# Kernel tuning notes

Measured on AMD Instinct MI355X. Metric: run time of the kernel, lower is better.

## Reference

```python
import jax, jax.numpy as jnp
import numpy as np

N, E, D_IN, H, OUT = 50000, 800000, 128, 256, 2
BN_EPS = 1e-5
LN_EPS = 1e-5


def _xavier(k, fi, fo):
    lim = float(np.sqrt(6.0 / (fi + fo)))
    return jax.random.uniform(k, (fi, fo), minval=-lim, maxval=lim, dtype=jnp.float32)


def setup_inputs() -> dict:
    key = jax.random.key(0)
    ks = jax.random.split(key, 8)
    return {
        "x": jax.random.normal(ks[0], (N, D_IN), dtype=jnp.float32),
        "edge_index": jax.random.randint(ks[1], (2, E), 0, N, dtype=jnp.int32),
        "feature_scale": jnp.ones((D_IN,), jnp.float32),
        "feature_bias": jnp.zeros((D_IN,), jnp.float32),
        "bn0_g": jnp.ones((D_IN,), jnp.float32),
        "bn0_b": jnp.zeros((D_IN,), jnp.float32),
        "W1": _xavier(ks[2], D_IN, H), "b1": jnp.zeros((H,), jnp.float32),
        "bn1_g": jnp.ones((H,), jnp.float32), "bn1_b": jnp.zeros((H,), jnp.float32),
        "ln1_g": jnp.ones((H,), jnp.float32), "ln1_b": jnp.zeros((H,), jnp.float32),
        "W2": _xavier(ks[3], H, H), "b2": jnp.zeros((H,), jnp.float32),
        "bn2_g": jnp.ones((H,), jnp.float32), "bn2_b": jnp.zeros((H,), jnp.float32),
        "ln2_g": jnp.ones((H,), jnp.float32), "ln2_b": jnp.zeros((H,), jnp.float32),
        "Wout": _xavier(ks[4], H, OUT), "bout": jnp.zeros((OUT,), jnp.float32),
    }


def _batchnorm(x, g, b):
    # training-mode BatchNorm1d: batch stats over node axis, biased variance
    mu = jnp.mean(x, axis=0)
    var = jnp.mean(jnp.square(x - mu), axis=0)
    return g * (x - mu) * jax.lax.rsqrt(var + BN_EPS) + b


def _layernorm(x, g, b):
    mu = jnp.mean(x, axis=-1, keepdims=True)
    var = jnp.mean(jnp.square(x - mu), axis=-1, keepdims=True)
    return g * (x - mu) * jax.lax.rsqrt(var + LN_EPS) + b


def _gcn(x, W, b, src, dst, dinv):
    # PyG GCNConv with self-loops: D^{-1/2}(A+I)D^{-1/2} X W + b
    h = x @ W                                   # [N, F]
    norm = (dinv[src] * dinv[dst])[:, None]     # [E, 1]
    msg = h[src] * norm                         # [E, F] (dominant traffic)
    agg = jax.ops.segment_sum(msg, dst, num_segments=N)
    return agg + (dinv * dinv)[:, None] * h + b


def _forward(x, feature_scale, feature_bias, bn0_g, bn0_b,
             W1, b1, bn1_g, bn1_b, ln1_g, ln1_b,
             W2, b2, bn2_g, bn2_b, ln2_g, ln2_b,
             Wout, bout, edge_index):
    src, dst = edge_index[0], edge_index[1]
    deg = jax.ops.segment_sum(jnp.ones((E,), x.dtype), dst, num_segments=N) + 1.0
    dinv = jax.lax.rsqrt(deg)

    h = x * feature_scale + feature_bias
    h = _batchnorm(h, bn0_g, bn0_b)            # input_bn; dropout = identity (eval)

    # layer 0 (no residual: i == 0)
    h1 = _gcn(h, W1, b1, src, dst, dinv)
    h1 = jax.nn.relu(h1)
    h1 = _batchnorm(h1, bn1_g, bn1_b)
    h1 = _layernorm(h1, ln1_g, ln1_b)

    # layer 1 (residual add, shapes match)
    h2 = _gcn(h1, W2, b2, src, dst, dinv)
    h2 = jax.nn.relu(h2)
    h2 = _batchnorm(h2, bn2_g, bn2_b)
    h2 = _layernorm(h2, ln2_g, ln2_b)
    h2 = h2 + h1

    return h2 @ Wout + bout


def reference(x, edge_index, feature_scale, feature_bias, bn0_g, bn0_b,
              W1, b1, bn1_g, bn1_b, ln1_g, ln1_b,
              W2, b2, bn2_g, bn2_b, ln2_g, ln2_b,
              Wout, bout):
    return _forward(x, feature_scale, feature_bias, bn0_g, bn0_b,
                    W1, b1, bn1_g, bn1_b, ln1_g, ln1_b,
                    W2, b2, bn2_g, bn2_b, ln2_g, ln2_b,
                    Wout, bout, edge_index)
```

## Files before the change

kernel.cpp:

```cpp
#include <hip/hip_runtime.h>
#include <hip/hip_bf16.h>
#include <stdint.h>

#define N_NODES 50000
#define N_EDGES 800000
#define D_IN    128
#define H_DIM   256
#define BN_EPS  1e-5f
#define LN_EPS  1e-5f
#define NBLK2 782
#define SLICE_ELEMS ((size_t)N_NODES * 32)
#define EDGE_CHUNK 4096
#define BN0_BLOCKS 1024
#define TR_BLOCKS 256
#define NBKT 196
#define CHUNK 2048
#define RCHUNKS 391

typedef float v4f __attribute__((ext_vector_type(4)));
typedef float v2f __attribute__((ext_vector_type(2)));
typedef short v8s __attribute__((ext_vector_type(8)));
typedef unsigned v4u __attribute__((ext_vector_type(4)));

__device__ __forceinline__ float bflo(unsigned u){ return __uint_as_float(u << 16); }
__device__ __forceinline__ float bfhi(unsigned u){ return __uint_as_float(u & 0xffff0000u); }
__device__ __forceinline__ unsigned short f2bf(float f){
  unsigned u = __float_as_uint(f);
  u += 0x7fffu + ((u >> 16) & 1u);
  return (unsigned short)(u >> 16);
}
__device__ __forceinline__ unsigned pack2(float a, float b){
  return (unsigned)f2bf(a) | ((unsigned)f2bf(b) << 16);
}

__device__ __forceinline__ int block_excl_scan(int v){
  int t = threadIdx.x;
  int lane = t & 63, w = t >> 6;
  int inc = v;
  #pragma unroll
  for (int m = 1; m < 64; m <<= 1){
    int o = __shfl_up(inc, m, 64);
    if (lane >= m) inc += o;
  }
  __shared__ int wsum[4];
  if (lane == 63) wsum[w] = inc;
  __syncthreads();
  int base = 0;
  #pragma unroll
  for (int j = 0; j < 4; ++j) if (j < w) base += wsum[j];
  return base + inc - v;
}

__global__ __launch_bounds__(256) void bn0r1_k(const int* ei, const float* x,
                                               const float* fs, const float* fb,
                                               float* S, float* Q, int* ghist){
  int b = blockIdx.x, t = threadIdx.x;
  if (b >= BN0_BLOCKS){
    __shared__ int lh[NBKT];
    int b2 = b - BN0_BLOCKS;
    for (int i = t; i < NBKT; i += 256) lh[i] = 0;
    __syncthreads();
    int e0 = b2 * CHUNK;
    int n = min(CHUNK, N_EDGES - e0);
    for (int i = t; i < n; i += 256)
      atomicAdd(&lh[ei[N_EDGES + e0 + i] >> 8], 1);
    __syncthreads();
    if (t < NBKT && lh[t] > 0) atomicAdd(&ghist[t], lh[t]);
    return;
  }
  int cl = t & 31, rg = t >> 5;
  int c = cl * 4;
  float4 fs4 = *(const float4*)(fs + c);
  float4 fb4 = *(const float4*)(fb + c);
  float s0=0,s1=0,s2=0,s3=0,q0=0,q1=0,q2=0,q3=0;
  for (int row = b * 8 + rg; row < N_NODES; row += BN0_BLOCKS * 8){
    float4 xv = *(const float4*)(x + (size_t)row * D_IN + c);
    float v0 = xv.x * fs4.x + fb4.x;
    float v1 = xv.y * fs4.y + fb4.y;
    float v2 = xv.z * fs4.z + fb4.z;
    float v3 = xv.w * fs4.w + fb4.w;
    s0 += v0; s1 += v1; s2 += v2; s3 += v3;
    q0 += v0*v0; q1 += v1*v1; q2 += v2*v2; q3 += v3*v3;
  }
  __shared__ float red[256][8];
  red[t][0]=s0; red[t][1]=s1; red[t][2]=s2; red[t][3]=s3;
  red[t][4]=q0; red[t][5]=q1; red[t][6]=q2; red[t][7]=q3;
  __syncthreads();
  float* Sr = S + (b & 7) * D_IN;
  float* Qr = Q + (b & 7) * D_IN;
  if (t < 32){
    float a[8];
    #pragma unroll
    for (int i = 0; i < 8; ++i) a[i] = red[t][i];
    for (int j = 1; j < 8; ++j)
      #pragma unroll
      for (int i = 0; i < 8; ++i) a[i] += red[t + 32*j][i];
    #pragma unroll
    for (int i = 0; i < 4; ++i){ atomicAdd(&Sr[t*4+i], a[i]); atomicAdd(&Qr[t*4+i], a[4+i]); }
  }
}

__global__ __launch_bounds__(256) void r3_k(const int* ei, const int* ghist, int* gcursor, unsigned* ebuf){
  __shared__ unsigned short dstS[CHUNK];
  __shared__ int lh[NBKT], cb[NBKT], sbb[NBKT];
  int t = threadIdx.x;
  int v = (t < NBKT) ? ghist[t] : 0;
  int epre = block_excl_scan(v);
  if (t < NBKT){ sbb[t] = epre; lh[t] = 0; }
  __syncthreads();
  int e0 = blockIdx.x * CHUNK;
  int n = min(CHUNK, N_EDGES - e0);
  for (int i = t; i < n; i += 256){
    int d = ei[N_EDGES + e0 + i];
    dstS[i] = (unsigned short)d;
    atomicAdd(&lh[d >> 8], 1);
  }
  __syncthreads();
  if (t < NBKT && lh[t] > 0) cb[t] = sbb[t] + atomicAdd(&gcursor[t], lh[t]);
  __syncthreads();
  if (t < NBKT) lh[t] = 0;
  __syncthreads();
  for (int i = t; i < n; i += 256){
    int d = dstS[i];
    int bkt = d >> 8;
    int r = atomicAdd(&lh[bkt], 1);
    unsigned src = (unsigned)ei[e0 + i];
    ebuf[cb[bkt] + r] = ((unsigned)(d & 255) << 16) | src;
  }
}

__global__ __launch_bounds__(256) void sortprep_k(const unsigned* ebuf, const int* ghist,
                                                  int* perm, int* offs, float* dinv,
                                                  unsigned short* edges,
                                                  const float* W1, const float* W2,
                                                  unsigned short* W1t, unsigned short* W2t){
  int b = blockIdx.x, t = threadIdx.x;
  if (b < NBKT){
    __shared__ int h[256], dh[128], ep_s[128], W_s[128], lc[128], curs[256], sbb[NBKT + 1];
    int gv = (t < NBKT) ? ghist[t] : 0;
    int gpre = block_excl_scan(gv);
    if (t < NBKT) sbb[t] = gpre;
    if (t == NBKT - 1) sbb[NBKT] = gpre + gv;
    h[t] = 0;
    if (t < 128){ dh[t] = 0; lc[t] = 0; }
    __syncthreads();
    int lo = sbb[b], hi = sbb[b + 1];
    for (int i = lo + t; i < hi; i += 256)
      atomicAdd(&h[(ebuf[i] >> 16) & 255], 1);
    __syncthreads();
    int node = b * 256 + t;
    bool valid = node < N_NODES;
    int deg = valid ? h[t] : 0;
    if (valid) atomicAdd(&dh[min(deg, 127)], 1);
    __syncthreads();
    int cv = (t < 128) ? dh[t] : 0;
    int e1 = block_excl_scan(cv);
    __syncthreads();
    int e2 = block_excl_scan((t < 128) ? cv * t : 0);
    __syncthreads();
    if (t < 128){ ep_s[t] = e1; W_s[t] = e2; }
    __syncthreads();
    if (valid){
      int bin = min(deg, 127);
      int r = atomicAdd(&lc[bin], 1);
      int pl = ep_s[bin] + r;
      int pos = b * 256 + pl;
      int off = lo + W_s[bin] + (pl - ep_s[bin]) * deg;
      perm[pos] = node;
      offs[pos] = off;
      dinv[node] = rsqrtf((float)deg + 1.0f);
      curs[t] = off;
    }
    __syncthreads();
    for (int i = lo + t; i < hi; i += 256){
      unsigned u = ebuf[i];
      int l8 = (u >> 16) & 255;
      int pos = atomicAdd(&curs[l8], 1);
      edges[pos] = (unsigned short)(u & 0xffffu);
    }
    if (b == 0 && t == 0) offs[N_NODES] = N_EDGES;
    return;
  }
  int i = (b - NBKT) * 256 + t;
  if (i < D_IN * H_DIM){
    int r = i / H_DIM, c = i % H_DIM;
    W1t[c * D_IN + r] = f2bf(W1[i]);
  }
  if (i < H_DIM * H_DIM){
    int r = i / H_DIM, c = i % H_DIM;
    W2t[c * H_DIM + r] = f2bf(W2[i]);
  }
}

__global__ __launch_bounds__(256) void gemm1_k(const float* x, const float* S, const float* Q,
                                               const float* fs, const float* fb,
                                               const float* gg, const float* bb,
                                               const unsigned short* Bt, const float* dinv,
                                               unsigned short* C, int M){
  __shared__ __align__(16) short smem[18944];
  __shared__ float ac[128], cc[128], dvs[64];
  short* As = smem;
  short* Bs = smem + 64 * 136;
  int t = threadIdx.x;
  int m0 = blockIdx.x * 64;
  int lane = t & 63, w = t >> 6;
  int fr = lane & 15, quad = lane >> 4;
  if (t < 64) dvs[t] = (m0 + t < M) ? dinv[m0 + t] : 0.0f;
  if (t < 128){
    float s8 = 0.f, q8 = 0.f;
    #pragma unroll
    for (int rep = 0; rep < 8; ++rep){ s8 += S[rep * D_IN + t]; q8 += Q[rep * D_IN + t]; }
    const float invN = 1.0f / N_NODES;
    float mu = s8 * invN;
    float rs = rsqrtf(q8 * invN - mu * mu + BN_EPS);
    float a = gg[t] * rs * fs[t];
    ac[t] = a;
    cc[t] = gg[t] * rs * (fb[t] - mu) + bb[t];
  }
  __syncthreads();
  {
    int r = t >> 2, q = t & 3;
    int arow = m0 + r;
    #pragma unroll
    for (int j = 0; j < 4; ++j){
      int c = q * 32 + j * 8;
      float4 xv0 = {0,0,0,0}, xv1 = {0,0,0,0};
      if (arow < M){
        xv0 = *(const float4*)(x + (size_t)arow * D_IN + c);
        xv1 = *(const float4*)(x + (size_t)arow * D_IN + c + 4);
      }
      float4 a0 = *(const float4*)(&ac[c]);
      float4 a1 = *(const float4*)(&ac[c + 4]);
      float4 c0 = *(const float4*)(&cc[c]);
      float4 c1 = *(const float4*)(&cc[c + 4]);
      uint4 o;
      o.x = pack2(a0.x * xv0.x + c0.x, a0.y * xv0.y + c0.y);
      o.y = pack2(a0.z * xv0.z + c0.z, a0.w * xv0.w + c0.w);
      o.z = pack2(a1.x * xv1.x + c1.x, a1.y * xv1.y + c1.y);
      o.w = pack2(a1.z * xv1.z + c1.z, a1.w * xv1.w + c1.w);
      *(uint4*)(&As[r * 136 + c]) = o;
    }
  }
  v4f acc[4][4] = {};
  int sr = t >> 2;
  int sk = (t & 3) << 3;
  for (int k0 = 0; k0 < D_IN; k0 += 32){
    __syncthreads();
    #pragma unroll
    for (int j = 0; j < 4; ++j){
      int brow = sr + 64 * j;
      uint4 bv = *(const uint4*)(Bt + (size_t)brow * D_IN + k0 + sk);
      *(uint4*)(&Bs[brow * 40 + sk]) = bv;
    }
    __syncthreads();
    v8s af[4], bf[4];
    #pragma unroll
    for (int mi = 0; mi < 4; ++mi)
      af[mi] = *(const v8s*)(&As[(mi * 16 + fr) * 136 + k0 + quad * 8]);
    #pragma unroll
    for (int ni = 0; ni < 4; ++ni)
      bf[ni] = *(const v8s*)(&Bs[(w * 64 + ni * 16 + fr) * 40 + quad * 8]);
    #pragma unroll
    for (int mi = 0; mi < 4; ++mi)
      #pragma unroll
      for (int ni = 0; ni < 4; ++ni)
        acc[mi][ni] = __builtin_amdgcn_mfma_f32_16x16x32_bf16(af[mi], bf[ni], acc[mi][ni], 0, 0, 0);
  }
  __syncthreads();
  short* Cs = smem;
  #pragma unroll
  for (int mi = 0; mi < 4; ++mi)
    #pragma unroll
    for (int ni = 0; ni < 4; ++ni)
      #pragma unroll
      for (int r = 0; r < 4; ++r){
        int row = mi * 16 + quad * 4 + r;
        int col = w * 64 + ni * 16 + fr;
        Cs[row * 264 + col] = (short)f2bf(acc[mi][ni][r] * dvs[row]);
      }
  __syncthreads();
  int orow = t >> 2;
  int grow = m0 + orow;
  if (grow < M){
    #pragma unroll
    for (int j = 0; j < 4; ++j){
      int oc = (t & 3) * 16 + 64 * j;
      v8s v0 = *(const v8s*)(&Cs[orow * 264 + oc]);
      v8s v1 = *(const v8s*)(&Cs[orow * 264 + oc + 8]);
      *(v8s*)(&C[(size_t)(oc >> 5) * SLICE_ELEMS + (size_t)grow * 32 + (oc & 31)]) = v0;
      int oc1 = oc + 8;
      *(v8s*)(&C[(size_t)(oc1 >> 5) * SLICE_ELEMS + (size_t)grow * 32 + (oc1 & 31)]) = v1;
    }
  }
}

__global__ __launch_bounds__(256) void gemm2_k(const unsigned short* gB,
                                               const float* Sg, const float* Qg,
                                               const float* bng, const float* bnb,
                                               const float* lng, const float* lnb,
                                               const unsigned short* Bt, const float* dinv,
                                               unsigned short* C, unsigned short* h1, int M){
  __shared__ __align__(16) short smem[16896];
  __shared__ float scs[256], shs[256], lgs[256], lbs[256], muS[64], rsS[64], dvs[64];
  short* As = smem;
  short* Bs = smem + 64 * 40;
  int t = threadIdx.x;
  int m0 = blockIdx.x * 64;
  int lane = t & 63, w = t >> 6;
  int fr = lane & 15, quad = lane >> 4;
  if (t < 64) dvs[t] = (m0 + t < M) ? dinv[m0 + t] : 0.0f;
  {
    const float invN = 1.0f / N_NODES;
    float mu = Sg[t] * invN;
    float rs = rsqrtf(Qg[t] * invN - mu * mu + BN_EPS);
    float s = bng[t] * rs;
    scs[t] = s; shs[t] = bnb[t] - s * mu;
    lgs[t] = lng[t]; lbs[t] = lnb[t];
  }
  __syncthreads();
  {
    int r = t >> 2, q = t & 3;
    int grow = m0 + r;
    float sum = 0.f, sq = 0.f;
    if (grow < M){
      #pragma unroll
      for (int j = 0; j < 8; ++j){
        int c = q * 64 + j * 8;
        uint4 u = *(const uint4*)(gB + (size_t)grow * H_DIM + c);
        float4 s0 = *(const float4*)(&scs[c]);
        float4 s1 = *(const float4*)(&scs[c + 4]);
        float4 h0 = *(const float4*)(&shs[c]);
        float4 h4 = *(const float4*)(&shs[c + 4]);
        float v0 = s0.x * bflo(u.x) + h0.x;
        float v1 = s0.y * bfhi(u.x) + h0.y;
        float v2 = s0.z * bflo(u.y) + h0.z;
        float v3 = s0.w * bfhi(u.y) + h0.w;
        float v4 = s1.x * bflo(u.z) + h4.x;
        float v5 = s1.y * bfhi(u.z) + h4.y;
        float v6 = s1.z * bflo(u.w) + h4.z;
        float v7 = s1.w * bfhi(u.w) + h4.w;
        sum += v0+v1+v2+v3+v4+v5+v6+v7;
        sq  += v0*v0+v1*v1+v2*v2+v3*v3+v4*v4+v5*v5+v6*v6+v7*v7;
      }
    }
    sum += __shfl_xor(sum, 1, 64); sum += __shfl_xor(sum, 2, 64);
    sq  += __shfl_xor(sq, 1, 64);  sq  += __shfl_xor(sq, 2, 64);
    if (q == 0){
      float mu = sum * (1.0f / H_DIM);
      float var = sq * (1.0f / H_DIM) - mu * mu;
      muS[r] = mu;
      rsS[r] = rsqrtf(var + LN_EPS);
    }
  }
  v4f acc[4][4] = {};
  int sr = t >> 2;
  int sk = (t & 3) << 3;
  for (int k0 = 0; k0 < H_DIM; k0 += 32){
    __syncthreads();
    {
      int arow = m0 + sr;
      uint4 av = {0,0,0,0};
      if (arow < M){
        int c = k0 + sk;
        uint4 u = *(const uint4*)(gB + (size_t)arow * H_DIM + c);
        float mu = muS[sr], rs = rsS[sr];
        float4 s0 = *(const float4*)(&scs[c]);
        float4 s1 = *(const float4*)(&scs[c + 4]);
        float4 h0 = *(const float4*)(&shs[c]);
        float4 h4 = *(const float4*)(&shs[c + 4]);
        float4 g0 = *(const float4*)(&lgs[c]);
        float4 g1 = *(const float4*)(&lgs[c + 4]);
        float4 b0 = *(const float4*)(&lbs[c]);
        float4 b1 = *(const float4*)(&lbs[c + 4]);
        float y0 = g0.x * ((s0.x * bflo(u.x) + h0.x) - mu) * rs + b0.x;
        float y1 = g0.y * ((s0.y * bfhi(u.x) + h0.y) - mu) * rs + b0.y;
        float y2 = g0.z * ((s0.z * bflo(u.y) + h0.z) - mu) * rs + b0.z;
        float y3 = g0.w * ((s0.w * bfhi(u.y) + h0.w) - mu) * rs + b0.w;
        float y4 = g1.x * ((s1.x * bflo(u.z) + h4.x) - mu) * rs + b1.x;
        float y5 = g1.y * ((s1.y * bfhi(u.z) + h4.y) - mu) * rs + b1.y;
        float y6 = g1.z * ((s1.z * bflo(u.w) + h4.z) - mu) * rs + b1.z;
        float y7 = g1.w * ((s1.w * bfhi(u.w) + h4.w) - mu) * rs + b1.w;
        av.x = pack2(y0, y1); av.y = pack2(y2, y3);
        av.z = pack2(y4, y5); av.w = pack2(y6, y7);
        *(uint4*)(h1 + (size_t)arow * H_DIM + c) = av;
      }
      *(uint4*)(&As[sr * 40 + sk]) = av;
    }
    #pragma unroll
    for (int j = 0; j < 4; ++j){
      int brow = sr + 64 * j;
      uint4 bv = *(const uint4*)(Bt + (size_t)brow * H_DIM + k0 + sk);
      *(uint4*)(&Bs[brow * 40 + sk]) = bv;
    }
    __syncthreads();
    v8s af[4], bf[4];
    #pragma unroll
    for (int mi = 0; mi < 4; ++mi)
      af[mi] = *(const v8s*)(&As[(mi * 16 + fr) * 40 + quad * 8]);
    #pragma unroll
    for (int ni = 0; ni < 4; ++ni)
      bf[ni] = *(const v8s*)(&Bs[(w * 64 + ni * 16 + fr) * 40 + quad * 8]);
    #pragma unroll
    for (int mi = 0; mi < 4; ++mi)
      #pragma unroll
      for (int ni = 0; ni < 4; ++ni)
        acc[mi][ni] = __builtin_amdgcn_mfma_f32_16x16x32_bf16(af[mi], bf[ni], acc[mi][ni], 0, 0, 0);
  }
  __syncthreads();
  short* Cs = smem;
  #pragma unroll
  for (int mi = 0; mi < 4; ++mi)
    #pragma unroll
    for (int ni = 0; ni < 4; ++ni)
      #pragma unroll
      for (int r = 0; r < 4; ++r){
        int row = mi * 16 + quad * 4 + r;
        int col = w * 64 + ni * 16 + fr;
        Cs[row * 264 + col] = (short)f2bf(acc[mi][ni][r] * dvs[row]);
      }
  __syncthreads();
  int orow = t >> 2;
  int grow = m0 + orow;
  if (grow < M){
    #pragma unroll
    for (int j = 0; j < 4; ++j){
      int oc = (t & 3) * 16 + 64 * j;
      v8s v0 = *(const v8s*)(&Cs[orow * 264 + oc]);
      v8s v1 = *(const v8s*)(&Cs[orow * 264 + oc + 8]);
      *(v8s*)(&C[(size_t)(oc >> 5) * SLICE_ELEMS + (size_t)grow * 32 + (oc & 31)]) = v0;
      int oc1 = oc + 8;
      *(v8s*)(&C[(size_t)(oc1 >> 5) * SLICE_ELEMS + (size_t)grow * 32 + (oc1 & 31)]) = v1;
    }
  }
}

#define ACCP(u, A) { v2f d_ = {bflo(u), bfhi(u)}; A += d_; }
#define ACC8(vv) ACCP(vv.x, A0) ACCP(vv.y, A1) ACCP(vv.z, A2) ACCP(vv.w, A3)

__global__ __launch_bounds__(256, 4) void agg_k(const unsigned short* hs, const int* offsets,
                                                const unsigned short* edges, const int* perm,
                                                const float* dinv, const float* bias,
                                                unsigned short* g, float* Sg, float* Qg){
  __shared__ unsigned eds32[EDGE_CHUNK / 2];
  __shared__ float wps[4][4][16];
  int t = threadIdx.x;
  int lane = t & 63;
  int wv = t >> 6;
  int slice = blockIdx.x & 7;
  int l4 = lane & 3;
  int grp = blockIdx.x >> 3;
  int nb = grp * 64;
  int idx = nb + (t >> 2);
  int lastn = min(nb + 64, N_NODES);
  int blk0 = offsets[nb];
  int base = blk0 & ~1;
  int blkN = offsets[lastn];
  const unsigned* gsrc = (const unsigned*)(edges + base);
  int nu = min((blkN - base + 1) >> 1, EDGE_CHUNK / 2);
  for (int i = t; i < nu; i += 256)
    eds32[i] = gsrc[i];
  __syncthreads();
  bool act = idx < N_NODES;
  int node = act ? perm[idx] : 0;
  float dvv = act ? dinv[node] : 0.f;
  const uint4* hb4 = (const uint4*)(hs + (size_t)slice * SLICE_ELEMS);
  float4 bb0 = *(const float4*)(bias + slice * 32 + l4 * 8);
  float4 bb1 = *(const float4*)(bias + slice * 32 + l4 * 8 + 4);
  uint4 sv = hb4[(size_t)node * 4 + l4];
  v2f A0 = {bflo(sv.x), bfhi(sv.x)};
  v2f A1 = {bflo(sv.y), bfhi(sv.y)};
  v2f A2 = {bflo(sv.z), bfhi(sv.z)};
  v2f A3 = {bflo(sv.w), bfhi(sv.w)};
  int e  = act ? offsets[idx] : 0;
  int e1 = act ? offsets[idx + 1] : 0;
  if ((e & 1) && e < e1){
    int ru = (e - base) >> 1;
    unsigned d = (ru < EDGE_CHUNK / 2) ? eds32[ru] : gsrc[ru];
    uint4 vv = hb4[(size_t)(d >> 16) * 4 + l4];
    ACC8(vv);
    ++e;
  }
  for (; e + 16 <= e1; e += 16){
    int ru = (e - base) >> 1;
    unsigned dd[8];
    if (ru + 8 <= EDGE_CHUNK / 2){
      #pragma unroll
      for (int j = 0; j < 8; ++j) dd[j] = eds32[ru + j];
    } else {
      #pragma unroll
      for (int j = 0; j < 8; ++j) dd[j] = gsrc[ru + j];
    }
    uint4 v[16];
    #pragma unroll
    for (int j = 0; j < 8; ++j){
      v[2*j]   = hb4[(size_t)(dd[j] & 0xffffu) * 4 + l4];
      v[2*j+1] = hb4[(size_t)(dd[j] >> 16)     * 4 + l4];
    }
    #pragma unroll
    for (int j = 0; j < 16; ++j){ ACC8(v[j]); }
  }
  if (e + 8 <= e1){
    int ru = (e - base) >> 1;
    unsigned dd[4];
    if (ru + 4 <= EDGE_CHUNK / 2){
      #pragma unroll
      for (int j = 0; j < 4; ++j) dd[j] = eds32[ru + j];
    } else {
      #pragma unroll
      for (int j = 0; j < 4; ++j) dd[j] = gsrc[ru + j];
    }
    uint4 v[8];
    #pragma unroll
    for (int j = 0; j < 4; ++j){
      v[2*j]   = hb4[(size_t)(dd[j] & 0xffffu) * 4 + l4];
      v[2*j+1] = hb4[(size_t)(dd[j] >> 16)     * 4 + l4];
    }
    #pragma unroll
    for (int j = 0; j < 8; ++j){ ACC8(v[j]); }
    e += 8;
  }
  if (e + 4 <= e1){
    int ru = (e - base) >> 1;
    unsigned dd0, dd1;
    if (ru + 2 <= EDGE_CHUNK / 2){
      dd0 = eds32[ru]; dd1 = eds32[ru + 1];
    } else {
      dd0 = gsrc[ru]; dd1 = gsrc[ru + 1];
    }
    uint4 v[4];
    v[0] = hb4[(size_t)(dd0 & 0xffffu) * 4 + l4];
    v[1] = hb4[(size_t)(dd0 >> 16)     * 4 + l4];
    v[2] = hb4[(size_t)(dd1 & 0xffffu) * 4 + l4];
    v[3] = hb4[(size_t)(dd1 >> 16)     * 4 + l4];
    #pragma unroll
    for (int j = 0; j < 4; ++j){ ACC8(v[j]); }
    e += 4;
  }
  for (; e < e1; ++e){
    int r = e - base;
    unsigned d = ((r >> 1) < EDGE_CHUNK / 2) ? eds32[r >> 1] : gsrc[r >> 1];
    unsigned s = (r & 1) ? (d >> 16) : (d & 0xffffu);
    uint4 vv = hb4[(size_t)s * 4 + l4];
    ACC8(vv);
  }
  float y0 = act ? fmaxf(dvv * A0.x + bb0.x, 0.f) : 0.f;
  float y1 = act ? fmaxf(dvv * A0.y + bb0.y, 0.f) : 0.f;
  float y2 = act ? fmaxf(dvv * A1.x + bb0.z, 0.f) : 0.f;
  float y3 = act ? fmaxf(dvv * A1.y + bb0.w, 0.f) : 0.f;
  float y4 = act ? fmaxf(dvv * A2.x + bb1.x, 0.f) : 0.f;
  float y5 = act ? fmaxf(dvv * A2.y + bb1.y, 0.f) : 0.f;
  float y6 = act ? fmaxf(dvv * A3.x + bb1.z, 0.f) : 0.f;
  float y7 = act ? fmaxf(dvv * A3.y + bb1.w, 0.f) : 0.f;
  if (act){
    v4u o;
    o.x = pack2(y0, y1); o.y = pack2(y2, y3);
    o.z = pack2(y4, y5); o.w = pack2(y6, y7);
    __builtin_nontemporal_store(o, (v4u*)(g + (size_t)node * H_DIM + slice * 32 + l4 * 8));
  }
  float q0 = y0*y0, q1 = y1*y1, q2 = y2*y2, q3 = y3*y3;
  float q4 = y4*y4, q5 = y5*y5, q6 = y6*y6, q7 = y7*y7;
  #pragma unroll
  for (int m = 4; m < 64; m <<= 1){
    y0 += __shfl_xor(y0, m, 64); y1 += __shfl_xor(y1, m, 64);
    y2 += __shfl_xor(y2, m, 64); y3 += __shfl_xor(y3, m, 64);
    y4 += __shfl_xor(y4, m, 64); y5 += __shfl_xor(y5, m, 64);
    y6 += __shfl_xor(y6, m, 64); y7 += __shfl_xor(y7, m, 64);
    q0 += __shfl_xor(q0, m, 64); q1 += __shfl_xor(q1, m, 64);
    q2 += __shfl_xor(q2, m, 64); q3 += __shfl_xor(q3, m, 64);
    q4 += __shfl_xor(q4, m, 64); q5 += __shfl_xor(q5, m, 64);
    q6 += __shfl_xor(q6, m, 64); q7 += __shfl_xor(q7, m, 64);
  }
  if (lane < 4){
    wps[wv][lane][0] = y0; wps[wv][lane][1] = y1; wps[wv][lane][2] = y2; wps[wv][lane][3] = y3;
    wps[wv][lane][4] = y4; wps[wv][lane][5] = y5; wps[wv][lane][6] = y6; wps[wv][lane][7] = y7;
    wps[wv][lane][8] = q0; wps[wv][lane][9] = q1; wps[wv][lane][10] = q2; wps[wv][lane][11] = q3;
    wps[wv][lane][12] = q4; wps[wv][lane][13] = q5; wps[wv][lane][14] = q6; wps[wv][lane][15] = q7;
  }
  __syncthreads();
  if (t < 64){
    int tl = t >> 4, ti = t & 15;
    float v = wps[0][tl][ti] + wps[1][tl][ti] + wps[2][tl][ti] + wps[3][tl][ti];
    int col32 = tl * 8 + (ti & 7);
    if (ti < 8) atomicAdd(&Sg[slice * 32 + col32], v);
    else        atomicAdd(&Qg[slice * 32 + col32], v);
  }
}

__global__ __launch_bounds__(256) void apply2_k(const unsigned short* g,
                                                const float* Sg, const float* Qg,
                                                const float* bng, const float* bnb,
                                                const float* lng, const float* lnb,
                                                const unsigned short* h1, const float* Wout,
                                                const float* bout, float* out){
  int t = threadIdx.x;
  int lane32 = t & 31;
  int row = blockIdx.x * 8 + (t >> 5);
  if (row >= N_NODES) return;
  int c = lane32 * 8;
  const float invN = 1.0f / N_NODES;
  float4 S0 = *(const float4*)(Sg + c), S1 = *(const float4*)(Sg + c + 4);
  float4 Q0 = *(const float4*)(Qg + c), Q1 = *(const float4*)(Qg + c + 4);
  float4 G0 = *(const float4*)(bng + c), G1 = *(const float4*)(bng + c + 4);
  float4 B0 = *(const float4*)(bnb + c), B1 = *(const float4*)(bnb + c + 4);
  float Sa[8] = {S0.x,S0.y,S0.z,S0.w,S1.x,S1.y,S1.z,S1.w};
  float Qa[8] = {Q0.x,Q0.y,Q0.z,Q0.w,Q1.x,Q1.y,Q1.z,Q1.w};
  float Ga[8] = {G0.x,G0.y,G0.z,G0.w,G1.x,G1.y,G1.z,G1.w};
  float Ba[8] = {B0.x,B0.y,B0.z,B0.w,B1.x,B1.y,B1.z,B1.w};
  float scv[8], shv[8];
  #pragma unroll
  for (int j = 0; j < 8; ++j){
    float mu = Sa[j] * invN;
    float rs = rsqrtf(Qa[j] * invN - mu * mu + BN_EPS);
    float s = Ga[j] * rs;
    scv[j] = s; shv[j] = Ba[j] - s * mu;
  }
  uint4 u = *(const uint4*)(g + (size_t)row * H_DIM + c);
  float v0 = scv[0] * bflo(u.x) + shv[0];
  float v1 = scv[1] * bfhi(u.x) + shv[1];
  float v2 = scv[2] * bflo(u.y) + shv[2];
  float v3 = scv[3] * bfhi(u.y) + shv[3];
  float v4 = scv[4] * bflo(u.z) + shv[4];
  float v5 = scv[5] * bfhi(u.z) + shv[5];
  float v6 = scv[6] * bflo(u.w) + shv[6];
  float v7 = scv[7] * bfhi(u.w) + shv[7];
  float sum = v0+v1+v2+v3+v4+v5+v6+v7;
  float sq  = v0*v0+v1*v1+v2*v2+v3*v3+v4*v4+v5*v5+v6*v6+v7*v7;
  #pragma unroll
  for (int m = 1; m < 32; m <<= 1){ sum += __shfl_xor(sum, m, 64); sq += __shfl_xor(sq, m, 64); }
  float mu = sum * (1.0f / H_DIM);
  float var = sq * (1.0f / H_DIM) - mu * mu;
  float rs = rsqrtf(var + LN_EPS);
  float4 g40 = *(const float4*)(lng + c);
  float4 g41 = *(const float4*)(lng + c + 4);
  float4 b40 = *(const float4*)(lnb + c);
  float4 b41 = *(const float4*)(lnb + c + 4);
  uint4 hr = *(const uint4*)(h1 + (size_t)row * H_DIM + c);
  float y0 = g40.x * (v0 - mu) * rs + b40.x + bflo(hr.x);
  float y1 = g40.y * (v1 - mu) * rs + b40.y + bfhi(hr.x);
  float y2 = g40.z * (v2 - mu) * rs + b40.z + bflo(hr.y);
  float y3 = g40.w * (v3 - mu) * rs + b40.w + bfhi(hr.y);
  float y4 = g41.x * (v4 - mu) * rs + b41.x + bflo(hr.z);
  float y5 = g41.y * (v5 - mu) * rs + b41.y + bfhi(hr.z);
  float y6 = g41.z * (v6 - mu) * rs + b41.z + bflo(hr.w);
  float y7 = g41.w * (v7 - mu) * rs + b41.w + bfhi(hr.w);
  float4 w0 = *(const float4*)(Wout + c * 2);
  float4 w1 = *(const float4*)(Wout + c * 2 + 4);
  float4 w2 = *(const float4*)(Wout + c * 2 + 8);
  float4 w3 = *(const float4*)(Wout + c * 2 + 12);
  float o0 = y0*w0.x + y1*w0.z + y2*w1.x + y3*w1.z + y4*w2.x + y5*w2.z + y6*w3.x + y7*w3.z;
  float o1 = y0*w0.y + y1*w0.w + y2*w1.y + y3*w1.w + y4*w2.y + y5*w2.w + y6*w3.y + y7*w3.w;
  #pragma unroll
  for (int m = 1; m < 32; m <<= 1){ o0 += __shfl_xor(o0, m, 64); o1 += __shfl_xor(o1, m, 64); }
  if (lane32 == 0){
    out[(size_t)row * 2 + 0] = o0 + bout[0];
    out[(size_t)row * 2 + 1] = o1 + bout[1];
  }
}

extern "C" void kernel_launch(void* const* d_in, const int* in_sizes, int n_in,
                              void* d_out, int out_size, void* d_ws, size_t ws_size,
                              hipStream_t stream) {
  const float* x    = (const float*)d_in[0];
  const int*   ei   = (const int*)d_in[1];
  const float* fs   = (const float*)d_in[2];
  const float* fb   = (const float*)d_in[3];
  const float* bn0g = (const float*)d_in[4];
  const float* bn0b = (const float*)d_in[5];
  const float* W1   = (const float*)d_in[6];
  const float* b1   = (const float*)d_in[7];
  const float* bn1g = (const float*)d_in[8];
  const float* bn1b = (const float*)d_in[9];
  const float* ln1g = (const float*)d_in[10];
  const float* ln1b = (const float*)d_in[11];
  const float* W2   = (const float*)d_in[12];
  const float* b2   = (const float*)d_in[13];
  const float* bn2g = (const float*)d_in[14];
  const float* bn2b = (const float*)d_in[15];
  const float* ln2g = (const float*)d_in[16];
  const float* ln2b = (const float*)d_in[17];
  const float* Wout = (const float*)d_in[18];
  const float* bout = (const float*)d_in[19];
  float* out = (float*)d_out;

  char* w = (char*)d_ws;
  float* bn0S  = (float*)(w + 0);
  float* bn0Q  = (float*)(w + 4096);
  int*   ghist  = (int*)(w + 8192);
  int*   gcursor= (int*)(w + 8976);
  float* Sg1   = (float*)(w + 9760);
  float* Qg1   = (float*)(w + 10784);
  float* Sg2   = (float*)(w + 11808);
  float* Qg2   = (float*)(w + 12832);
  const size_t ZERO_BYTES = 13856;
  float* dinv  = (float*)(w + 211584);
  int*   offs  = (int*)(w + 411584);
  int*   perm  = (int*)(w + 611712);
  unsigned short* edges = (unsigned short*)(w + 1011712);
  unsigned short* W1t  = (unsigned short*)(w + 15411712);
  unsigned short* W2t  = (unsigned short*)(w + 15477248);
  unsigned short* hlin = (unsigned short*)(w + 15608320);
  unsigned*       ebuf = (unsigned*)(w + 15608320);
  unsigned short* gbuf = (unsigned short*)(w + 41208320);
  unsigned short* h1   = (unsigned short*)(w + 66808320);

  (void)in_sizes; (void)n_in; (void)out_size; (void)ws_size;

  hipMemsetAsync(d_ws, 0, ZERO_BYTES, stream);

  bn0r1_k<<<BN0_BLOCKS + RCHUNKS, 256, 0, stream>>>(ei, x, fs, fb, bn0S, bn0Q, ghist);
  r3_k<<<RCHUNKS, 256, 0, stream>>>(ei, ghist, gcursor, ebuf);
  sortprep_k<<<NBKT + TR_BLOCKS, 256, 0, stream>>>(
      ebuf, ghist, perm, offs, dinv, edges, W1, W2, W1t, W2t);

  int ggrid = (N_NODES + 63) / 64;
  int agg_blocks = NBLK2 * 8;

  gemm1_k<<<ggrid, 256, 0, stream>>>(x, bn0S, bn0Q, fs, fb, bn0g, bn0b, W1t, dinv, hlin, N_NODES);
  agg_k<<<agg_blocks, 256, 0, stream>>>(hlin, offs, edges, perm, dinv, b1, gbuf, Sg1, Qg1);

  gemm2_k<<<ggrid, 256, 0, stream>>>(gbuf, Sg1, Qg1, bn1g, bn1b, ln1g, ln1b, W2t, dinv, hlin, h1, N_NODES);
  agg_k<<<agg_blocks, 256, 0, stream>>>(hlin, offs, edges, perm, dinv, b2, gbuf, Sg2, Qg2);
  apply2_k<<<(N_NODES + 7) / 8, 256, 0, stream>>>(gbuf, Sg2, Qg2, bn2g, bn2b, ln2g, ln2b, h1, Wout, bout, out);
}
```

Before: 334.6 us.

## Enlarge gemm1 tile to 128 rows with 8 waves and stream A per k-step

gemm1 now processes 128 rows per block with 512 threads arranged as a 2x4 wave grid. Each block loads W1 tiles once for twice as many rows, which halves B-operand traffic. The A operand (BN-normalized x) is converted per 32-wide k-chunk instead of staging the whole row up front, so shared memory shrinks. The epilogue writes the output in two 64-row halves through shared memory with wider contiguous stores. The cost is half as many blocks, which lowers occupancy, plus extra barriers in the epilogue.

```diff
diff --git a/kernel.cpp b/kernel.cpp
--- a/kernel.cpp
+++ b/kernel.cpp
@@ -192,21 +192,22 @@
   }
 }
 
-__global__ __launch_bounds__(256) void gemm1_k(const float* x, const float* S, const float* Q,
+__global__ __launch_bounds__(512) void gemm1_k(const float* x, const float* S, const float* Q,
                                                const float* fs, const float* fb,
                                                const float* gg, const float* bb,
                                                const unsigned short* Bt, const float* dinv,
                                                unsigned short* C, int M){
-  __shared__ __align__(16) short smem[18944];
-  __shared__ float ac[128], cc[128], dvs[64];
+  __shared__ __align__(16) short smem[16896];
+  __shared__ float ac[128], cc[128], dvs[128];
   short* As = smem;
-  short* Bs = smem + 64 * 136;
+  short* Bs = smem + 128 * 40;
   int t = threadIdx.x;
-  int m0 = blockIdx.x * 64;
+  int m0 = blockIdx.x * 128;
   int lane = t & 63, w = t >> 6;
+  int wr = w >> 2, wc = w & 3;
   int fr = lane & 15, quad = lane >> 4;
-  if (t < 64) dvs[t] = (m0 + t < M) ? dinv[m0 + t] : 0.0f;
   if (t < 128){
+    dvs[t] = (m0 + t < M) ? dinv[m0 + t] : 0.0f;
     float s8 = 0.f, q8 = 0.f;
     #pragma unroll
     for (int rep = 0; rep < 8; ++rep){ s8 += S[rep * D_IN + t]; q8 += Q[rep * D_IN + t]; }
@@ -218,12 +219,14 @@
     cc[t] = gg[t] * rs * (fb[t] - mu) + bb[t];
   }
   __syncthreads();
-  {
-    int r = t >> 2, q = t & 3;
-    int arow = m0 + r;
-    #pragma unroll
-    for (int j = 0; j < 4; ++j){
-      int c = q * 32 + j * 8;
+  v4f acc[4][4] = {};
+  int ar = t >> 2, aq = t & 3;
+  int br = t >> 1, bh = t & 1;
+  for (int k0 = 0; k0 < D_IN; k0 += 32){
+    __syncthreads();
+    {
+      int arow = m0 + ar;
+      int c = k0 + aq * 8;
       float4 xv0 = {0,0,0,0}, xv1 = {0,0,0,0};
       if (arow < M){
         xv0 = *(const float4*)(x + (size_t)arow * D_IN + c);
@@ -238,58 +241,59 @@
       o.y = pack2(a0.z * xv0.z + c0.z, a0.w * xv0.w + c0.w);
       o.z = pack2(a1.x * xv1.x + c1.x, a1.y * xv1.y + c1.y);
       o.w = pack2(a1.z * xv1.z + c1.z, a1.w * xv1.w + c1.w);
-      *(uint4*)(&As[r * 136 + c]) = o;
-    }
-  }
-  v4f acc[4][4] = {};
-  int sr = t >> 2;
-  int sk = (t & 3) << 3;
-  for (int k0 = 0; k0 < D_IN; k0 += 32){
-    __syncthreads();
-    #pragma unroll
-    for (int j = 0; j < 4; ++j){
-      int brow = sr + 64 * j;
-      uint4 bv = *(const uint4*)(Bt + (size_t)brow * D_IN + k0 + sk);
-      *(uint4*)(&Bs[brow * 40 + sk]) = bv;
+      *(uint4*)(&As[ar * 40 + aq * 8]) = o;
+    }
+    {
+      const unsigned short* bp = Bt + (size_t)br * D_IN + k0 + bh * 16;
+      uint4 b0 = *(const uint4*)(bp);
+      uint4 b1 = *(const uint4*)(bp + 8);
+      *(uint4*)(&Bs[br * 40 + bh * 16]) = b0;
+      *(uint4*)(&Bs[br * 40 + bh * 16 + 8]) = b1;
     }
     __syncthreads();
     v8s af[4], bf[4];
     #pragma unroll
     for (int mi = 0; mi < 4; ++mi)
-      af[mi] = *(const v8s*)(&As[(mi * 16 + fr) * 136 + k0 + quad * 8]);
+      af[mi] = *(const v8s*)(&As[(wr * 64 + mi * 16 + fr) * 40 + quad * 8]);
     #pragma unroll
     for (int ni = 0; ni < 4; ++ni)
-      bf[ni] = *(const v8s*)(&Bs[(w * 64 + ni * 16 + fr) * 40 + quad * 8]);
+      bf[ni] = *(const v8s*)(&Bs[(wc * 64 + ni * 16 + fr) * 40 + quad * 8]);
     #pragma unroll
     for (int mi = 0; mi < 4; ++mi)
       #pragma unroll
       for (int ni = 0; ni < 4; ++ni)
         acc[mi][ni] = __builtin_amdgcn_mfma_f32_16x16x32_bf16(af[mi], bf[ni], acc[mi][ni], 0, 0, 0);
   }
-  __syncthreads();
   short* Cs = smem;
   #pragma unroll
-  for (int mi = 0; mi < 4; ++mi)
-    #pragma unroll
-    for (int ni = 0; ni < 4; ++ni)
-      #pragma unroll
-      for (int r = 0; r < 4; ++r){
-        int row = mi * 16 + quad * 4 + r;
-        int col = w * 64 + ni * 16 + fr;
-        Cs[row * 264 + col] = (short)f2bf(acc[mi][ni][r] * dvs[row]);
-      }
-  __syncthreads();
-  int orow = t >> 2;
-  int grow = m0 + orow;
-  if (grow < M){
-    #pragma unroll
-    for (int j = 0; j < 4; ++j){
-      int oc = (t & 3) * 16 + 64 * j;
-      v8s v0 = *(const v8s*)(&Cs[orow * 264 + oc]);
-      v8s v1 = *(const v8s*)(&Cs[orow * 264 + oc + 8]);
-      *(v8s*)(&C[(size_t)(oc >> 5) * SLICE_ELEMS + (size_t)grow * 32 + (oc & 31)]) = v0;
-      int oc1 = oc + 8;
-      *(v8s*)(&C[(size_t)(oc1 >> 5) * SLICE_ELEMS + (size_t)grow * 32 + (oc1 & 31)]) = v1;
+  for (int h = 0; h < 2; ++h){
+    __syncthreads();
+    if (wr == h){
+      #pragma unroll
+      for (int mi = 0; mi < 4; ++mi)
+        #pragma unroll
+        for (int ni = 0; ni < 4; ++ni)
+          #pragma unroll
+          for (int r = 0; r < 4; ++r){
+            int row = mi * 16 + quad * 4 + r;
+            int col = wc * 64 + ni * 16 + fr;
+            Cs[row * 264 + col] = (short)f2bf(acc[mi][ni][r] * dvs[h * 64 + row]);
+          }
+    }
+    __syncthreads();
+    int orow = t >> 3, o8 = t & 7;
+    int grow = m0 + h * 64 + orow;
+    if (grow < M){
+      const short* src = &Cs[orow * 264 + o8 * 32];
+      unsigned short* dst = C + (size_t)o8 * SLICE_ELEMS + (size_t)grow * 32;
+      v8s v0 = *(const v8s*)(src);
+      v8s v1 = *(const v8s*)(src + 8);
+      v8s v2 = *(const v8s*)(src + 16);
+      v8s v3 = *(const v8s*)(src + 24);
+      *(v8s*)(dst) = v0;
+      *(v8s*)(dst + 8) = v1;
+      *(v8s*)(dst + 16) = v2;
+      *(v8s*)(dst + 24) = v3;
     }
   }
 }
@@ -712,13 +716,14 @@
   sortprep_k<<<NBKT + TR_BLOCKS, 256, 0, stream>>>(
       ebuf, ghist, perm, offs, dinv, edges, W1, W2, W1t, W2t);
 
-  int ggrid = (N_NODES + 63) / 64;
+  int g1grid = (N_NODES + 127) / 128;
+  int g2grid = (N_NODES + 63) / 64;
   int agg_blocks = NBLK2 * 8;
 
-  gemm1_k<<<ggrid, 256, 0, stream>>>(x, bn0S, bn0Q, fs, fb, bn0g, bn0b, W1t, dinv, hlin, N_NODES);
+  gemm1_k<<<g1grid, 512, 0, stream>>>(x, bn0S, bn0Q, fs, fb, bn0g, bn0b, W1t, dinv, hlin, N_NODES);
   agg_k<<<agg_blocks, 256, 0, stream>>>(hlin, offs, edges, perm, dinv, b1, gbuf, Sg1, Qg1);
 
-  gemm2_k<<<ggrid, 256, 0, stream>>>(gbuf, Sg1, Qg1, bn1g, bn1b, ln1g, ln1b, W2t, dinv, hlin, h1, N_NODES);
+  gemm2_k<<<g2grid, 256, 0, stream>>>(gbuf, Sg1, Qg1, bn1g, bn1b, ln1g, ln1b, W2t, dinv, hlin, h1, N_NODES);
   agg_k<<<agg_blocks, 256, 0, stream>>>(hlin, offs, edges, perm, dinv, b2, gbuf, Sg2, Qg2);
   apply2_k<<<(N_NODES + 7) / 8, 256, 0, stream>>>(gbuf, Sg2, Qg2, bn2g, bn2b, ln2g, ln2b, h1, Wout, bout, out);
 }
```

New measurement: 330.7 us, median of 2. Within noise of the previous version (-1.2%).
